# Performance work log

Measured on AMD Instinct MI355X. Metric: run time of the kernel, lower is better.

Reference implementation:

```python
import jax, jax.numpy as jnp
import numpy as np

IMG_W = 256.0  # image_size[0]
IMG_H = 256.0  # image_size[1]


def setup_inputs() -> dict:
    key = jax.random.key(0)
    x = jax.random.normal(key, (64, 34, 256, 256), dtype=jnp.float32)
    return {"x": x}


def reference(x):
    B, C, W, H = x.shape
    k = C // 2
    N = W * H
    xf = x.reshape(B, C, N)
    h = xf[:, :k]          # heatmaps  [B, k, N]
    v = xf[:, k:]          # uncertainty maps [B, k, N]
    w = jax.nn.softmax(h, axis=-1)                     # softmax over spatial dim
    p = jnp.arange(N, dtype=x.dtype)                   # position index vector
    ki = jnp.round(jnp.sum(w * p, axis=-1))            # soft-argmax, rounded (float, grad 0)
    co_x = jnp.mod(ki, W) / W * IMG_W                  # ki % width / width * imgsz[0]
    co_y = jnp.floor(ki / W) / H * IMG_H               # ki // width / height * imgsz[1]
    vi = jnp.sum(w * v, axis=-1)                       # confidence = sum(softmax * uncertainty)
    return jnp.stack([co_x, co_y, vi], axis=-1)        # [B, k, 3]
```

## Files before the change

kernel.cpp:

```cpp
#include <hip/hip_runtime.h>
#include <hip/hip_bf16.h>


#define KD_K 17
#define KD_C 34
#define KD_N 65536
#define KD_N4 (KD_N / 4)
#define KD_THREADS 256

__global__ __launch_bounds__(KD_THREADS)
void kd_kernel(const float* __restrict__ x, float* __restrict__ out) {
    const int pair = blockIdx.x;
    const int b = pair / KD_K;
    const int c = pair % KD_K;

    const float4* __restrict__ h4 =
        reinterpret_cast<const float4*>(x + (size_t)(b * KD_C + c) * KD_N);
    const float4* __restrict__ v4 =
        reinterpret_cast<const float4*>(x + (size_t)(b * KD_C + c + KD_K) * KD_N);

    double s = 0.0, sp = 0.0, sv = 0.0;

    #pragma unroll 4
    for (int j = threadIdx.x; j < KD_N4; j += KD_THREADS) {
        const float4 h = h4[j];
        const float4 v = v4[j];
        const float e0 = expf(h.x);
        const float e1 = expf(h.y);
        const float e2 = expf(h.z);
        const float e3 = expf(h.w);
        const double i0 = (double)(4 * j);
        s  += ((double)e0 + (double)e1) + ((double)e2 + (double)e3);
        sp += ((double)e0 * i0 + (double)e1 * (i0 + 1.0)) +
              ((double)e2 * (i0 + 2.0) + (double)e3 * (i0 + 3.0));
        sv += ((double)e0 * (double)v.x + (double)e1 * (double)v.y) +
              ((double)e2 * (double)v.z + (double)e3 * (double)v.w);
    }

    #pragma unroll
    for (int off = 32; off > 0; off >>= 1) {
        s  += __shfl_xor(s,  off);
        sp += __shfl_xor(sp, off);
        sv += __shfl_xor(sv, off);
    }

    __shared__ double ls[3][4];
    const int wid  = threadIdx.x >> 6;
    const int lane = threadIdx.x & 63;
    if (lane == 0) {
        ls[0][wid] = s;
        ls[1][wid] = sp;
        ls[2][wid] = sv;
    }
    __syncthreads();

    if (threadIdx.x == 0) {
        const double S  = (ls[0][0] + ls[0][1]) + (ls[0][2] + ls[0][3]);
        const double SP = (ls[1][0] + ls[1][1]) + (ls[1][2] + ls[1][3]);
        const double SV = (ls[2][0] + ls[2][1]) + (ls[2][2] + ls[2][3]);

        const double ki   = rint(SP / S);
        const double row  = floor(ki * (1.0 / 256.0));
        const double co_x = ki - 256.0 * row;
        const double co_y = row;

        float* o = out + (size_t)(b * KD_K + c) * 3;
        o[0] = (float)co_x;
        o[1] = (float)co_y;
        o[2] = (float)(SV / S);
    }
}

extern "C" void kernel_launch(void* const* d_in, const int* in_sizes, int n_in,
                              void* d_out, int out_size, void* d_ws, size_t ws_size,
                              hipStream_t stream) {
    const float* x = (const float*)d_in[0];
    float* out = (float*)d_out;
    kd_kernel<<<dim3(64 * KD_K), dim3(KD_THREADS), 0, stream>>>(x, out);
}
```

Before: 710.5 us.

## Split each spatial reduction across two blocks with a second combine kernel

Each (batch, keypoint) reduction is split into two halves handled by separate blocks, which write partial double sums to workspace. A second small kernel adds the halves and computes the coordinates and confidence. Loads also become nontemporal. The aim is more blocks in flight (2176 instead of 1088) to saturate HBM bandwidth, at the cost of an extra kernel launch and a workspace round trip.

```diff
diff --git a/kernel.cpp b/kernel.cpp
--- a/kernel.cpp
+++ b/kernel.cpp
@@ -5,31 +5,40 @@
 #define KD_K 17
 #define KD_C 34
 #define KD_N 65536
-#define KD_N4 (KD_N / 4)
+#define KD_SPLIT 2
+#define KD_HALF_N  (KD_N / KD_SPLIT)
+#define KD_HALF_N4 (KD_HALF_N / 4)
 #define KD_THREADS 256
+#define KD_UNITS  (64 * KD_K)
+#define KD_BLOCKS1 (KD_UNITS * KD_SPLIT)
+
+typedef float f32x4 __attribute__((ext_vector_type(4)));
 
 __global__ __launch_bounds__(KD_THREADS)
-void kd_kernel(const float* __restrict__ x, float* __restrict__ out) {
-    const int pair = blockIdx.x;
-    const int b = pair / KD_K;
-    const int c = pair % KD_K;
+void kd_stage1(const float* __restrict__ x, double* __restrict__ ws) {
+    const int blk  = blockIdx.x;
+    const int unit = blk / KD_SPLIT;
+    const int half = blk % KD_SPLIT;
+    const int b = unit / KD_K;
+    const int c = unit % KD_K;
 
-    const float4* __restrict__ h4 =
-        reinterpret_cast<const float4*>(x + (size_t)(b * KD_C + c) * KD_N);
-    const float4* __restrict__ v4 =
-        reinterpret_cast<const float4*>(x + (size_t)(b * KD_C + c + KD_K) * KD_N);
+    const f32x4* __restrict__ h4 = reinterpret_cast<const f32x4*>(
+        x + (size_t)(b * KD_C + c) * KD_N + half * KD_HALF_N);
+    const f32x4* __restrict__ v4 = reinterpret_cast<const f32x4*>(
+        x + (size_t)(b * KD_C + c + KD_K) * KD_N + half * KD_HALF_N);
+    const int elem0 = half * KD_HALF_N;
 
     double s = 0.0, sp = 0.0, sv = 0.0;
 
     #pragma unroll 4
-    for (int j = threadIdx.x; j < KD_N4; j += KD_THREADS) {
-        const float4 h = h4[j];
-        const float4 v = v4[j];
+    for (int j = threadIdx.x; j < KD_HALF_N4; j += KD_THREADS) {
+        const f32x4 h = __builtin_nontemporal_load(h4 + j);
+        const f32x4 v = __builtin_nontemporal_load(v4 + j);
         const float e0 = expf(h.x);
         const float e1 = expf(h.y);
         const float e2 = expf(h.z);
         const float e3 = expf(h.w);
-        const double i0 = (double)(4 * j);
+        const double i0 = (double)(elem0 + 4 * j);
         s  += ((double)e0 + (double)e1) + ((double)e2 + (double)e3);
         sp += ((double)e0 * i0 + (double)e1 * (i0 + 1.0)) +
               ((double)e2 * (i0 + 2.0) + (double)e3 * (i0 + 3.0));
@@ -55,20 +64,31 @@
     __syncthreads();
 
     if (threadIdx.x == 0) {
-        const double S  = (ls[0][0] + ls[0][1]) + (ls[0][2] + ls[0][3]);
-        const double SP = (ls[1][0] + ls[1][1]) + (ls[1][2] + ls[1][3]);
-        const double SV = (ls[2][0] + ls[2][1]) + (ls[2][2] + ls[2][3]);
+        double* w = ws + (size_t)blk * 4;
+        w[0] = (ls[0][0] + ls[0][1]) + (ls[0][2] + ls[0][3]);
+        w[1] = (ls[1][0] + ls[1][1]) + (ls[1][2] + ls[1][3]);
+        w[2] = (ls[2][0] + ls[2][1]) + (ls[2][2] + ls[2][3]);
+    }
+}
 
-        const double ki   = rint(SP / S);
-        const double row  = floor(ki * (1.0 / 256.0));
-        const double co_x = ki - 256.0 * row;
-        const double co_y = row;
+__global__ __launch_bounds__(KD_THREADS)
+void kd_stage2(const double* __restrict__ ws, float* __restrict__ out) {
+    const int u = blockIdx.x * KD_THREADS + threadIdx.x;
+    if (u >= KD_UNITS) return;
 
-        float* o = out + (size_t)(b * KD_K + c) * 3;
-        o[0] = (float)co_x;
-        o[1] = (float)co_y;
-        o[2] = (float)(SV / S);
-    }
+    const double* w = ws + (size_t)u * KD_SPLIT * 4;
+    const double S  = w[0] + w[4];
+    const double SP = w[1] + w[5];
+    const double SV = w[2] + w[6];
+
+    const double ki   = rint(SP / S);
+    const double row  = floor(ki * (1.0 / 256.0));
+    const double co_x = ki - 256.0 * row;
+
+    float* o = out + (size_t)u * 3;
+    o[0] = (float)co_x;
+    o[1] = (float)row;
+    o[2] = (float)(SV / S);
 }
 
 extern "C" void kernel_launch(void* const* d_in, const int* in_sizes, int n_in,
@@ -76,5 +96,9 @@
                               hipStream_t stream) {
     const float* x = (const float*)d_in[0];
     float* out = (float*)d_out;
-    kd_kernel<<<dim3(64 * KD_K), dim3(KD_THREADS), 0, stream>>>(x, out);
+    double* ws = (double*)d_ws;
+
+    kd_stage1<<<dim3(KD_BLOCKS1), dim3(KD_THREADS), 0, stream>>>(x, ws);
+    kd_stage2<<<dim3((KD_UNITS + KD_THREADS - 1) / KD_THREADS),
+                dim3(KD_THREADS), 0, stream>>>(ws, out);
 }
```

Result: faster. 693.7 us (-2.4%).
